# Performance work log

Measured on AMD Instinct MI355X. Metric: run time of the kernel, lower is better.

Reference implementation:

```python
import jax, jax.numpy as jnp
import numpy as np

H = 16  # num heads
D = 64  # head dim


def rotate_half(x):
    h = x.shape[-1] // 2
    return jnp.concatenate([-x[..., h:], x[..., :h]], axis=-1)


def setup_inputs() -> dict:
    key = jax.random.key(0)
    ks = jax.random.split(key, 8)
    B, S, E = 2, 4096, 1024
    scale = 1.0 / np.sqrt(E)
    x = jax.random.normal(ks[0], (B, S, E), dtype=jnp.float32)
    Wq = jax.random.normal(ks[1], (E, E), dtype=jnp.float32) * scale
    Wk = jax.random.normal(ks[2], (E, E), dtype=jnp.float32) * scale
    Wv = jax.random.normal(ks[3], (E, E), dtype=jnp.float32) * scale
    Wg = jax.random.normal(ks[4], (E, E), dtype=jnp.float32) * scale
    Wo = jax.random.normal(ks[5], (E, E), dtype=jnp.float32) * scale
    cos = jax.random.normal(ks[6], (S, D), dtype=jnp.float32)
    sin = jax.random.normal(ks[7], (S, D), dtype=jnp.float32)
    return {"x": x, "Wq": Wq, "Wk": Wk, "Wv": Wv, "Wg": Wg, "Wo": Wo,
            "cos": cos, "sin": sin, "block_size": 256}


def reference(x, Wq, Wk, Wv, Wg, Wo, cos, sin, block_size):
    B, S, E = x.shape
    nb = S // block_size  # seq divisible by block_size (remainder==0 path)

    gate = (x @ Wg).reshape(B, S, H, D)
    q = (x @ Wq).reshape(B, S, H, D)
    k = (x @ Wk).reshape(B, S, H, D)
    v = (x @ Wv).reshape(B, S, H, D)

    # RoPE: cos/sin [S, D] -> broadcast over batch and heads (unsqueeze_dim=1 in torch
    # with [S, 1, D] after slicing gives the same broadcast over the head axis here).
    c = cos[:S][None, :, None, :]  # [1, S, 1, D]
    s = sin[:S][None, :, None, :]
    q = q * c + rotate_half(q) * s
    k = k * c + rotate_half(k) * s

    # Block-diagonal attention: reshape seq into blocks and attend within blocks only.
    def to_blocks(t):  # [B,S,H,D] -> [B,nb,H,block,D]
        return t.reshape(B, nb, block_size, H, D).transpose(0, 1, 3, 2, 4)

    qb, kb, vb = to_blocks(q), to_blocks(k), to_blocks(v)
    scores = jnp.einsum('bnhqd,bnhkd->bnhqk', qb, kb) / np.sqrt(D)
    attn = jax.nn.softmax(scores, axis=-1)
    ob = jnp.einsum('bnhqk,bnhkd->bnhqd', attn, vb)

    out = ob.transpose(0, 1, 3, 2, 4).reshape(B, S, H, D)  # back to [B,S,H,D]
    out = (out * jax.nn.sigmoid(gate)).reshape(B, S, H * D)
    return out @ Wo
```

## Files before the change

### kernel.cpp

```cpp
#include <hip/hip_runtime.h>
#include <hip/hip_bf16.h>
#include <stdint.h>

typedef __bf16 bf16_t;
typedef __bf16 bf16x8 __attribute__((ext_vector_type(8)));
typedef float f32x4 __attribute__((ext_vector_type(4)));

#define DEVI __device__ __forceinline__

constexpr int BB = 2;
constexpr int SS = 4096;
constexpr int EE = 1024;
constexpr int HH = 16;
constexpr int DD = 64;
constexpr int MM = BB * SS;

DEVI void gload16(const void* g, void* l) {
  __builtin_amdgcn_global_load_lds(
      (const __attribute__((address_space(1))) void*)g,
      (__attribute__((address_space(3))) void*)l, 16, 0, 0);
}

__global__ void cvt_kernel(const float* __restrict__ in, bf16_t* __restrict__ out, int n8) {
  int i = blockIdx.x * 256 + threadIdx.x;
  if (i >= n8) return;
  const float* p = in + (size_t)i * 8;
  bf16x8 o;
#pragma unroll
  for (int j = 0; j < 8; ++j) o[j] = (bf16_t)p[j];
  *(bf16x8*)(out + (size_t)i * 8) = o;
}

__global__ void wt_kernel(const float* __restrict__ w0, const float* __restrict__ w1,
                          const float* __restrict__ w2, const float* __restrict__ w3,
                          const float* __restrict__ w4, bf16_t* __restrict__ out) {
  __shared__ float tile[32][33];
  const float* Wsel = blockIdx.z == 0 ? w0 : blockIdx.z == 1 ? w1 :
                      blockIdx.z == 2 ? w2 : blockIdx.z == 3 ? w3 : w4;
  bf16_t* O = out + (size_t)blockIdx.z * EE * EE;
  int n0 = blockIdx.x * 32, k0 = blockIdx.y * 32;
  int tx = threadIdx.x & 31, ty = threadIdx.x >> 5;
#pragma unroll
  for (int i = 0; i < 4; ++i)
    tile[ty + i * 8][tx] = Wsel[(size_t)(k0 + ty + i * 8) * EE + n0 + tx];
  __syncthreads();
#pragma unroll
  for (int i = 0; i < 4; ++i)
    O[(size_t)(n0 + ty + i * 8) * EE + k0 + tx] = (bf16_t)tile[tx][ty + i * 8];
}

template <int MODE>
__global__ __launch_bounds__(256) void gemm_bt(const bf16_t* __restrict__ A,
                                               const bf16_t* __restrict__ Bt,
                                               void* __restrict__ Cout, int Kdim) {
  __shared__ bf16_t Al[128 * 64];
  __shared__ bf16_t Bl[128 * 64];
  const int m0 = blockIdx.x * 128;
  const int n0 = blockIdx.y * 128;
  const int tid = threadIdx.x;
  const int wv = tid >> 6, ln = tid & 63;
  const int wm = wv >> 1, wn = wv & 1;
  f32x4 acc[4][4] = {};

  for (int k0 = 0; k0 < Kdim; k0 += 64) {
    __syncthreads();
#pragma unroll
    for (int i = 0; i < 4; ++i) {
      int slot = i * 256 + wv * 64 + ln;
      int r = slot >> 3, c = slot & 7;
      int cs = c ^ (r & 7);
      gload16(A + (size_t)(m0 + r) * Kdim + k0 + cs * 8, Al + (size_t)(i * 256 + wv * 64) * 8);
      gload16(Bt + (size_t)(n0 + r) * Kdim + k0 + cs * 8, Bl + (size_t)(i * 256 + wv * 64) * 8);
    }
    __syncthreads();
#pragma unroll
    for (int kk = 0; kk < 2; ++kk) {
      bf16x8 af[4], bfr[4];
#pragma unroll
      for (int mi = 0; mi < 4; ++mi) {
        int row = wm * 64 + mi * 16 + (ln & 15);
        int ch = (kk * 4 + (ln >> 4)) ^ (row & 7);
        af[mi] = *(const bf16x8*)(Al + row * 64 + ch * 8);
      }
#pragma unroll
      for (int ni = 0; ni < 4; ++ni) {
        int row = wn * 64 + ni * 16 + (ln & 15);
        int ch = (kk * 4 + (ln >> 4)) ^ (row & 7);
        bfr[ni] = *(const bf16x8*)(Bl + row * 64 + ch * 8);
      }
#pragma unroll
      for (int mi = 0; mi < 4; ++mi)
#pragma unroll
        for (int ni = 0; ni < 4; ++ni)
          acc[mi][ni] = __builtin_amdgcn_mfma_f32_16x16x32_bf16(af[mi], bfr[ni], acc[mi][ni], 0, 0, 0);
    }
  }

  if (MODE == 0) {
    bf16_t* Obase = (bf16_t*)Cout;
#pragma unroll
    for (int mi = 0; mi < 4; ++mi) {
#pragma unroll
      for (int ni = 0; ni < 4; ++ni) {
        int row = m0 + wm * 64 + mi * 16 + ((ln >> 4) << 2);
        int col = n0 + wn * 64 + ni * 16 + (ln & 15);
        int widx = col >> 10, ncol = col & 1023;
        bf16_t* W = Obase + (size_t)widx * MM * EE;
        if (widx == 2) {
          int h = ncol >> 6, d = ncol & 63;
          int b = row >> 12, s = row & (SS - 1);
          bf16_t* p = W + (((size_t)b * HH + h) * DD + d) * SS + s;
#pragma unroll
          for (int r = 0; r < 4; ++r) p[r] = (bf16_t)acc[mi][ni][r];
        } else {
          bf16_t* p = W + (size_t)row * EE + ncol;
#pragma unroll
          for (int r = 0; r < 4; ++r) p[(size_t)r * EE] = (bf16_t)acc[mi][ni][r];
        }
      }
    }
  } else {
    float* O = (float*)Cout;
#pragma unroll
    for (int mi = 0; mi < 4; ++mi)
#pragma unroll
      for (int ni = 0; ni < 4; ++ni) {
        int row = m0 + wm * 64 + mi * 16 + ((ln >> 4) << 2);
        int col = n0 + wn * 64 + ni * 16 + (ln & 15);
#pragma unroll
        for (int r = 0; r < 4; ++r) O[(size_t)(row + r) * EE + col] = acc[mi][ni][r];
      }
  }
}

__global__ __launch_bounds__(256, 2) void attn_kernel(const bf16_t* __restrict__ Q,
                                                      const bf16_t* __restrict__ Kc,
                                                      const bf16_t* __restrict__ Vt,
                                                      const bf16_t* __restrict__ G,
                                                      const float* __restrict__ cosp,
                                                      const float* __restrict__ sinp,
                                                      bf16_t* __restrict__ AO) {
  __shared__ bf16_t Kl[256 * 64];
  __shared__ bf16_t Vl[64 * 256];
  __shared__ bf16_t Pl[4][32 * 64];
  const int id = blockIdx.x;
  const int swz = (id & 7) * 128 + (id >> 3);
  const int half = swz & 1, ab = swz >> 1;
  const int h = ab & 15, sb = (ab >> 4) & 15, b = ab >> 8;
  const int tid = threadIdx.x, wv = tid >> 6, ln = tid & 63;
  const int qs0 = sb * 256 + half * 128 + wv * 32;

  {
    const bf16_t* Kbase = Kc + ((size_t)b * SS + sb * 256) * EE + h * DD;
    int kr = wv * 8 + (ln >> 3), kc8 = ln & 7;
#pragma unroll
    for (int g = 0; g < 8; ++g) {
      int r = g * 32 + kr, cs = kc8 ^ (r & 7);
      gload16(Kbase + (size_t)r * EE + cs * 8, &Kl[g * 2048 + wv * 512]);
    }
    const bf16_t* Vbase = Vt + ((size_t)b * HH + h) * DD * SS + sb * 256;
    int vr = wv * 2 + (ln >> 5), vc = ln & 31;
#pragma unroll
    for (int g = 0; g < 8; ++g) {
      int r = g * 8 + vr, cs = vc ^ ((r & 7) << 2);
      gload16(Vbase + (size_t)r * SS + cs * 8, &Vl[g * 2048 + wv * 512]);
    }
  }

  const int erow = ln >> 1, ehf = ln & 1;
  const int em = b * SS + qs0 + erow;
  bf16x8 gpre[4];
  {
    const bf16_t* gp = G + (size_t)em * EE + h * DD + ehf * 32;
#pragma unroll
    for (int i = 0; i < 4; ++i) gpre[i] = *(const bf16x8*)(gp + i * 8);
  }

  bf16x8 qraw[2][2];
  float cl[2][8], sl[2][8], chv[2][8], shv[2][8];
  const int d0 = (ln >> 4) << 3;
#pragma unroll
  for (int mi = 0; mi < 2; ++mi) {
    int qs = qs0 + mi * 16 + (ln & 15);
    const bf16_t* qp = Q + ((size_t)b * SS + qs) * EE + h * DD;
    qraw[mi][0] = *(const bf16x8*)(qp + d0);
    qraw[mi][1] = *(const bf16x8*)(qp + 32 + d0);
    *(f32x4*)&cl[mi][0] = *(const f32x4*)&cosp[qs * DD + d0];
    *(f32x4*)&cl[mi][4] = *(const f32x4*)&cosp[qs * DD + d0 + 4];
    *(f32x4*)&chv[mi][0] = *(const f32x4*)&cosp[qs * DD + d0 + 32];
    *(f32x4*)&chv[mi][4] = *(const f32x4*)&cosp[qs * DD + d0 + 36];
    *(f32x4*)&sl[mi][0] = *(const f32x4*)&sinp[qs * DD + d0];
    *(f32x4*)&sl[mi][4] = *(const f32x4*)&sinp[qs * DD + d0 + 4];
    *(f32x4*)&shv[mi][0] = *(const f32x4*)&sinp[qs * DD + d0 + 32];
    *(f32x4*)&shv[mi][4] = *(const f32x4*)&sinp[qs * DD + d0 + 36];
  }
  __syncthreads();

  bf16x8 qf[2][2];
#pragma unroll
  for (int mi = 0; mi < 2; ++mi)
#pragma unroll
    for (int j = 0; j < 8; ++j) {
      float lo = (float)qraw[mi][0][j], hi = (float)qraw[mi][1][j];
      qf[mi][0][j] = (bf16_t)(lo * cl[mi][j] - hi * sl[mi][j]);
      qf[mi][1][j] = (bf16_t)(hi * chv[mi][j] + lo * shv[mi][j]);
    }

  {
    int c_ = tid & 3;
#pragma unroll
    for (int rr = 0; rr < 4; ++rr) {
      int r_ = rr * 64 + (tid >> 2);
      int ks = sb * 256 + r_;
      int chl = ((c_ ^ (r_ & 7)) << 3), chh = (((c_ ^ 4) ^ (r_ & 7)) << 3);
      bf16x8 lo8 = *(bf16x8*)&Kl[r_ * 64 + chl];
      bf16x8 hi8 = *(bf16x8*)&Kl[r_ * 64 + chh];
      float kc_[8], ks_[8], kch[8], ksh[8];
      *(f32x4*)&kc_[0] = *(const f32x4*)&cosp[ks * DD + c_ * 8];
      *(f32x4*)&kc_[4] = *(const f32x4*)&cosp[ks * DD + c_ * 8 + 4];
      *(f32x4*)&kch[0] = *(const f32x4*)&cosp[ks * DD + c_ * 8 + 32];
      *(f32x4*)&kch[4] = *(const f32x4*)&cosp[ks * DD + c_ * 8 + 36];
      *(f32x4*)&ks_[0] = *(const f32x4*)&sinp[ks * DD + c_ * 8];
      *(f32x4*)&ks_[4] = *(const f32x4*)&sinp[ks * DD + c_ * 8 + 4];
      *(f32x4*)&ksh[0] = *(const f32x4*)&sinp[ks * DD + c_ * 8 + 32];
      *(f32x4*)&ksh[4] = *(const f32x4*)&sinp[ks * DD + c_ * 8 + 36];
      bf16x8 olo, ohi;
#pragma unroll
      for (int j = 0; j < 8; ++j) {
        float lo = (float)lo8[j], hi = (float)hi8[j];
        olo[j] = (bf16_t)(lo * kc_[j] - hi * ks_[j]);
        ohi[j] = (bf16_t)(hi * kch[j] + lo * ksh[j]);
      }
      *(bf16x8*)&Kl[r_ * 64 + chl] = olo;
      *(bf16x8*)&Kl[r_ * 64 + chh] = ohi;
    }
  }
  __syncthreads();

  f32x4 sc[2][16];
#pragma unroll
  for (int mi = 0; mi < 2; ++mi)
#pragma unroll
    for (int ni = 0; ni < 16; ++ni) sc[mi][ni] = f32x4{0.f, 0.f, 0.f, 0.f};
  __builtin_amdgcn_s_setprio(1);
#pragma unroll
  for (int kk = 0; kk < 2; ++kk) {
#pragma unroll
    for (int ni = 0; ni < 16; ++ni) {
      int row = ni * 16 + (ln & 15);
      int ch = (kk * 4 + (ln >> 4)) ^ (row & 7);
      bf16x8 kf = *(const bf16x8*)(&Kl[row * 64 + ch * 8]);
#pragma unroll
      for (int mi = 0; mi < 2; ++mi)
        sc[mi][ni] = __builtin_amdgcn_mfma_f32_16x16x32_bf16(qf[mi][kk], kf, sc[mi][ni], 0, 0, 0);
    }
  }
  __builtin_amdgcn_s_setprio(0);

  float lr[2][4];
#pragma unroll
  for (int mi = 0; mi < 2; ++mi) {
#pragma unroll
    for (int r = 0; r < 4; ++r) {
      float mx = -1e30f;
#pragma unroll
      for (int ni = 0; ni < 16; ++ni) mx = fmaxf(mx, sc[mi][ni][r] * 0.125f);
#pragma unroll
      for (int d = 1; d < 16; d <<= 1) mx = fmaxf(mx, __shfl_xor(mx, d));
      float rs = 0.f;
#pragma unroll
      for (int ni = 0; ni < 16; ++ni) {
        float p = __expf(sc[mi][ni][r] * 0.125f - mx);
        sc[mi][ni][r] = p;
        rs += p;
      }
#pragma unroll
      for (int d = 1; d < 16; d <<= 1) rs += __shfl_xor(rs, d);
      lr[mi][r] = rs;
    }
  }

  f32x4 o[2][4] = {};
  bf16_t* P = Pl[wv];
#pragma unroll
  for (int kc = 0; kc < 4; ++kc) {
#pragma unroll
    for (int mi = 0; mi < 2; ++mi)
#pragma unroll
      for (int nq = 0; nq < 4; ++nq)
#pragma unroll
        for (int r = 0; r < 4; ++r) {
          int row = mi * 16 + ((ln >> 4) << 2) + r;
          int col = nq * 16 + (ln & 15);
          P[row * 64 + (col ^ ((row & 7) << 3))] = (bf16_t)sc[mi][kc * 4 + nq][r];
        }
    __builtin_amdgcn_s_setprio(1);
#pragma unroll
    for (int kk = 0; kk < 2; ++kk) {
      bf16x8 pf[2], vf[4];
#pragma unroll
      for (int mi = 0; mi < 2; ++mi) {
        int row = mi * 16 + (ln & 15);
        int ch = (kk * 4 + (ln >> 4)) ^ (row & 7);
        pf[mi] = *(const bf16x8*)(P + row * 64 + ch * 8);
      }
#pragma unroll
      for (int nd = 0; nd < 4; ++nd) {
        int d = nd * 16 + (ln & 15);
        int c = (kc * 8 + kk * 4 + (ln >> 4)) ^ ((d & 7) << 2);
        vf[nd] = *(const bf16x8*)(&Vl[d * 256 + c * 8]);
      }
#pragma unroll
      for (int mi = 0; mi < 2; ++mi)
#pragma unroll
        for (int nd = 0; nd < 4; ++nd)
          o[mi][nd] = __builtin_amdgcn_mfma_f32_16x16x32_bf16(pf[mi], vf[nd], o[mi][nd], 0, 0, 0);
    }
    __builtin_amdgcn_s_setprio(0);
  }

  __syncthreads();
  float* lrT = (float*)Pl[wv];
  if ((ln & 15) == 0) {
#pragma unroll
    for (int mi = 0; mi < 2; ++mi)
#pragma unroll
      for (int r = 0; r < 4; ++r)
        lrT[mi * 16 + ((ln >> 4) << 2) + r] = lr[mi][r];
  }
  float* T = (float*)Kl + wv * 2048;
#pragma unroll
  for (int mi = 0; mi < 2; ++mi)
#pragma unroll
    for (int nd = 0; nd < 4; ++nd)
#pragma unroll
      for (int r = 0; r < 4; ++r) {
        int row = mi * 16 + ((ln >> 4) << 2) + r;
        int col = nd * 16 + (ln & 15);
        int c = col >> 2;
        T[row * 64 + ((c ^ (row & 7)) << 2) + (col & 3)] = o[mi][nd][r];
      }
  {
    float inv = 1.f / lrT[erow];
    f32x4 ov[8];
#pragma unroll
    for (int j = 0; j < 8; ++j) {
      int c = ehf * 8 + j;
      ov[j] = *(const f32x4*)&T[erow * 64 + ((c ^ (erow & 7)) << 2)];
    }
    bf16_t* ap = AO + (size_t)em * EE + h * DD + ehf * 32;
#pragma unroll
    for (int i = 0; i < 4; ++i) {
      bf16x8 outv;
#pragma unroll
      for (int j2 = 0; j2 < 8; ++j2) {
        float gv = (float)gpre[i][j2];
        float sig = 1.f / (1.f + __expf(-gv));
        outv[j2] = (bf16_t)(ov[i * 2 + (j2 >> 2)][j2 & 3] * inv * sig);
      }
      *(bf16x8*)(ap + i * 8) = outv;
    }
  }
}

extern "C" void kernel_launch(void* const* d_in, const int* in_sizes, int n_in,
                              void* d_out, int out_size, void* d_ws, size_t ws_size,
                              hipStream_t stream) {
  const float* x = (const float*)d_in[0];
  const float* Wq = (const float*)d_in[1];
  const float* Wk = (const float*)d_in[2];
  const float* Wv = (const float*)d_in[3];
  const float* Wg = (const float*)d_in[4];
  const float* Wo = (const float*)d_in[5];
  const float* cosp = (const float*)d_in[6];
  const float* sinp = (const float*)d_in[7];
  float* out = (float*)d_out;

  char* ws = (char*)d_ws;
  bf16_t* XB = (bf16_t*)(ws);
  bf16_t* WT = (bf16_t*)(ws + (16ll << 20));
  bf16_t* QB = (bf16_t*)(ws + (26ll << 20));
  bf16_t* KB = (bf16_t*)(ws + (42ll << 20));
  bf16_t* VT = (bf16_t*)(ws + (58ll << 20));
  bf16_t* GB = (bf16_t*)(ws + (74ll << 20));
  bf16_t* AO = XB;

  const int n8 = MM * EE / 8;
  cvt_kernel<<<n8 / 256, 256, 0, stream>>>(x, XB, n8);
  wt_kernel<<<dim3(32, 32, 5), 256, 0, stream>>>(Wq, Wk, Wv, Wg, Wo, WT);
  gemm_bt<0><<<dim3(MM / 128, 4 * EE / 128), 256, 0, stream>>>(XB, WT, QB, EE);
  attn_kernel<<<1024, 256, 0, stream>>>(QB, KB, VT, GB, cosp, sinp, AO);
  gemm_bt<1><<<dim3(MM / 128, EE / 128), 256, 0, stream>>>(AO, WT + (size_t)4 * EE * EE, out, EE);
}
```

Baseline: 155.0 us.

## Pack RoPE cos/sin to bf16 and split K/V load waits in attention

Adds a small pre-kernel that rewrites the cos/sin tables into an interleaved bf16 layout, so each thread fetches its RoPE coefficients in a few 16-byte loads instead of many fp32 loads. The attention kernel now issues those loads first, then the K and V async LDS loads, and waits only for the K loads (vmcnt(8)) before applying RoPE to K. It waits for V only right before the PV stage, so the V transfer can overlap the QK and softmax work. The cost is an extra tiny launch and bf16 rounding of cos/sin. The hand-written waitcnt counts depend on the exact instruction order, which makes the code fragile.

```diff
diff --git a/kernel.cpp b/kernel.cpp
--- a/kernel.cpp
+++ b/kernel.cpp
@@ -47,6 +47,17 @@
 #pragma unroll
   for (int i = 0; i < 4; ++i)
     O[(size_t)(n0 + ty + i * 8) * EE + k0 + tx] = (bf16_t)tile[tx][ty + i * 8];
+}
+
+__global__ void csk_kernel(const float* __restrict__ cosp, const float* __restrict__ sinp,
+                           bf16_t* __restrict__ csk) {
+  int i = blockIdx.x * 256 + threadIdx.x;
+  int s = i >> 7, idx = i & 127;
+  int c = idx >> 5, j = idx & 31;
+  int part = j >> 3, jj = j & 7;
+  int d = c * 8 + jj + ((part >= 2) ? 32 : 0);
+  const float* src = (part & 1) ? sinp : cosp;
+  csk[i] = (bf16_t)src[s * 64 + d];
 }
 
 template <int MODE>
@@ -137,8 +148,7 @@
                                                       const bf16_t* __restrict__ Kc,
                                                       const bf16_t* __restrict__ Vt,
                                                       const bf16_t* __restrict__ G,
-                                                      const float* __restrict__ cosp,
-                                                      const float* __restrict__ sinp,
+                                                      const bf16_t* __restrict__ CSK,
                                                       bf16_t* __restrict__ AO) {
   __shared__ bf16_t Kl[256 * 64];
   __shared__ bf16_t Vl[64 * 256];
@@ -150,23 +160,27 @@
   const int tid = threadIdx.x, wv = tid >> 6, ln = tid & 63;
   const int qs0 = sb * 256 + half * 128 + wv * 32;
 
-  {
-    const bf16_t* Kbase = Kc + ((size_t)b * SS + sb * 256) * EE + h * DD;
-    int kr = wv * 8 + (ln >> 3), kc8 = ln & 7;
-#pragma unroll
-    for (int g = 0; g < 8; ++g) {
-      int r = g * 32 + kr, cs = kc8 ^ (r & 7);
-      gload16(Kbase + (size_t)r * EE + cs * 8, &Kl[g * 2048 + wv * 512]);
-    }
-    const bf16_t* Vbase = Vt + ((size_t)b * HH + h) * DD * SS + sb * 256;
-    int vr = wv * 2 + (ln >> 5), vc = ln & 31;
-#pragma unroll
-    for (int g = 0; g < 8; ++g) {
-      int r = g * 8 + vr, cs = vc ^ ((r & 7) << 2);
-      gload16(Vbase + (size_t)r * SS + cs * 8, &Vl[g * 2048 + wv * 512]);
-    }
-  }
-
+  const int d0 = (ln >> 4) << 3;
+  bf16x8 qraw[2][2], qcs[2][4];
+#pragma unroll
+  for (int mi = 0; mi < 2; ++mi) {
+    int qs = qs0 + mi * 16 + (ln & 15);
+    const bf16_t* qp = Q + ((size_t)b * SS + qs) * EE + h * DD;
+    qraw[mi][0] = *(const bf16x8*)(qp + d0);
+    qraw[mi][1] = *(const bf16x8*)(qp + 32 + d0);
+    const bf16_t* cp = CSK + (size_t)qs * 128 + (d0 >> 3) * 32;
+#pragma unroll
+    for (int t = 0; t < 4; ++t) qcs[mi][t] = *(const bf16x8*)(cp + t * 8);
+  }
+  const int kcol = tid & 3;
+  bf16x8 kcs[4][4];
+#pragma unroll
+  for (int rr = 0; rr < 4; ++rr) {
+    int ks = sb * 256 + rr * 64 + (tid >> 2);
+    const bf16_t* cp = CSK + (size_t)ks * 128 + kcol * 32;
+#pragma unroll
+    for (int t = 0; t < 4; ++t) kcs[rr][t] = *(const bf16x8*)(cp + t * 8);
+  }
   const int erow = ln >> 1, ehf = ln & 1;
   const int em = b * SS + qs0 + erow;
   bf16x8 gpre[4];
@@ -175,26 +189,29 @@
 #pragma unroll
     for (int i = 0; i < 4; ++i) gpre[i] = *(const bf16x8*)(gp + i * 8);
   }
-
-  bf16x8 qraw[2][2];
-  float cl[2][8], sl[2][8], chv[2][8], shv[2][8];
-  const int d0 = (ln >> 4) << 3;
-#pragma unroll
-  for (int mi = 0; mi < 2; ++mi) {
-    int qs = qs0 + mi * 16 + (ln & 15);
-    const bf16_t* qp = Q + ((size_t)b * SS + qs) * EE + h * DD;
-    qraw[mi][0] = *(const bf16x8*)(qp + d0);
-    qraw[mi][1] = *(const bf16x8*)(qp + 32 + d0);
-    *(f32x4*)&cl[mi][0] = *(const f32x4*)&cosp[qs * DD + d0];
-    *(f32x4*)&cl[mi][4] = *(const f32x4*)&cosp[qs * DD + d0 + 4];
-    *(f32x4*)&chv[mi][0] = *(const f32x4*)&cosp[qs * DD + d0 + 32];
-    *(f32x4*)&chv[mi][4] = *(const f32x4*)&cosp[qs * DD + d0 + 36];
-    *(f32x4*)&sl[mi][0] = *(const f32x4*)&sinp[qs * DD + d0];
-    *(f32x4*)&sl[mi][4] = *(const f32x4*)&sinp[qs * DD + d0 + 4];
-    *(f32x4*)&shv[mi][0] = *(const f32x4*)&sinp[qs * DD + d0 + 32];
-    *(f32x4*)&shv[mi][4] = *(const f32x4*)&sinp[qs * DD + d0 + 36];
-  }
-  __syncthreads();
+  __builtin_amdgcn_sched_barrier(0);
+
+  {
+    const bf16_t* Kbase = Kc + ((size_t)b * SS + sb * 256) * EE + h * DD;
+    int kr = wv * 8 + (ln >> 3), kc8 = ln & 7;
+#pragma unroll
+    for (int g = 0; g < 8; ++g) {
+      int r = g * 32 + kr, cs = kc8 ^ (r & 7);
+      gload16(Kbase + (size_t)r * EE + cs * 8, &Kl[g * 2048 + wv * 512]);
+    }
+  }
+  __builtin_amdgcn_sched_barrier(0);
+
+  {
+    const bf16_t* Vbase = Vt + ((size_t)b * HH + h) * DD * SS + sb * 256;
+    int vr = wv * 2 + (ln >> 5), vc = ln & 31;
+#pragma unroll
+    for (int g = 0; g < 8; ++g) {
+      int r = g * 8 + vr, cs = vc ^ ((r & 7) << 2);
+      gload16(Vbase + (size_t)r * SS + cs * 8, &Vl[g * 2048 + wv * 512]);
+    }
+  }
+  __builtin_amdgcn_sched_barrier(0);
 
   bf16x8 qf[2][2];
 #pragma unroll
@@ -202,40 +219,34 @@
 #pragma unroll
     for (int j = 0; j < 8; ++j) {
       float lo = (float)qraw[mi][0][j], hi = (float)qraw[mi][1][j];
-      qf[mi][0][j] = (bf16_t)(lo * cl[mi][j] - hi * sl[mi][j]);
-      qf[mi][1][j] = (bf16_t)(hi * chv[mi][j] + lo * shv[mi][j]);
-    }
-
-  {
-    int c_ = tid & 3;
-#pragma unroll
-    for (int rr = 0; rr < 4; ++rr) {
-      int r_ = rr * 64 + (tid >> 2);
-      int ks = sb * 256 + r_;
-      int chl = ((c_ ^ (r_ & 7)) << 3), chh = (((c_ ^ 4) ^ (r_ & 7)) << 3);
-      bf16x8 lo8 = *(bf16x8*)&Kl[r_ * 64 + chl];
-      bf16x8 hi8 = *(bf16x8*)&Kl[r_ * 64 + chh];
-      float kc_[8], ks_[8], kch[8], ksh[8];
-      *(f32x4*)&kc_[0] = *(const f32x4*)&cosp[ks * DD + c_ * 8];
-      *(f32x4*)&kc_[4] = *(const f32x4*)&cosp[ks * DD + c_ * 8 + 4];
-      *(f32x4*)&kch[0] = *(const f32x4*)&cosp[ks * DD + c_ * 8 + 32];
-      *(f32x4*)&kch[4] = *(const f32x4*)&cosp[ks * DD + c_ * 8 + 36];
-      *(f32x4*)&ks_[0] = *(const f32x4*)&sinp[ks * DD + c_ * 8];
-      *(f32x4*)&ks_[4] = *(const f32x4*)&sinp[ks * DD + c_ * 8 + 4];
-      *(f32x4*)&ksh[0] = *(const f32x4*)&sinp[ks * DD + c_ * 8 + 32];
-      *(f32x4*)&ksh[4] = *(const f32x4*)&sinp[ks * DD + c_ * 8 + 36];
-      bf16x8 olo, ohi;
-#pragma unroll
-      for (int j = 0; j < 8; ++j) {
-        float lo = (float)lo8[j], hi = (float)hi8[j];
-        olo[j] = (bf16_t)(lo * kc_[j] - hi * ks_[j]);
-        ohi[j] = (bf16_t)(hi * kch[j] + lo * ksh[j]);
-      }
-      *(bf16x8*)&Kl[r_ * 64 + chl] = olo;
-      *(bf16x8*)&Kl[r_ * 64 + chh] = ohi;
-    }
-  }
-  __syncthreads();
+      qf[mi][0][j] = (bf16_t)(lo * (float)qcs[mi][0][j] - hi * (float)qcs[mi][1][j]);
+      qf[mi][1][j] = (bf16_t)(hi * (float)qcs[mi][2][j] + lo * (float)qcs[mi][3][j]);
+    }
+
+  asm volatile("s_waitcnt vmcnt(8)" ::: "memory");
+  __builtin_amdgcn_s_barrier();
+  __builtin_amdgcn_sched_barrier(0);
+
+#pragma unroll
+  for (int rr = 0; rr < 4; ++rr) {
+    int r_ = rr * 64 + (tid >> 2);
+    int chl = ((kcol ^ (r_ & 7)) << 3), chh = (((kcol ^ 4) ^ (r_ & 7)) << 3);
+    bf16x8 lo8 = *(bf16x8*)&Kl[r_ * 64 + chl];
+    bf16x8 hi8 = *(bf16x8*)&Kl[r_ * 64 + chh];
+    bf16x8 olo, ohi;
+#pragma unroll
+    for (int j = 0; j < 8; ++j) {
+      float lo = (float)lo8[j], hi = (float)hi8[j];
+      olo[j] = (bf16_t)(lo * (float)kcs[rr][0][j] - hi * (float)kcs[rr][1][j]);
+      ohi[j] = (bf16_t)(hi * (float)kcs[rr][2][j] + lo * (float)kcs[rr][3][j]);
+    }
+    *(bf16x8*)&Kl[r_ * 64 + chl] = olo;
+    *(bf16x8*)&Kl[r_ * 64 + chh] = ohi;
+  }
+
+  asm volatile("s_waitcnt lgkmcnt(0)" ::: "memory");
+  __builtin_amdgcn_s_barrier();
+  __builtin_amdgcn_sched_barrier(0);
 
   f32x4 sc[2][16];
 #pragma unroll
@@ -279,6 +290,10 @@
       lr[mi][r] = rs;
     }
   }
+
+  asm volatile("s_waitcnt vmcnt(0)" ::: "memory");
+  __builtin_amdgcn_s_barrier();
+  __builtin_amdgcn_sched_barrier(0);
 
   f32x4 o[2][4] = {};
   bf16_t* P = Pl[wv];
@@ -383,12 +398,14 @@
   bf16_t* KB = (bf16_t*)(ws + (42ll << 20));
   bf16_t* VT = (bf16_t*)(ws + (58ll << 20));
   bf16_t* GB = (bf16_t*)(ws + (74ll << 20));
+  bf16_t* CK = (bf16_t*)(ws + (90ll << 20));
   bf16_t* AO = XB;
 
   const int n8 = MM * EE / 8;
   cvt_kernel<<<n8 / 256, 256, 0, stream>>>(x, XB, n8);
   wt_kernel<<<dim3(32, 32, 5), 256, 0, stream>>>(Wq, Wk, Wv, Wg, Wo, WT);
+  csk_kernel<<<(SS * 128) / 256, 256, 0, stream>>>(cosp, sinp, CK);
   gemm_bt<0><<<dim3(MM / 128, 4 * EE / 128), 256, 0, stream>>>(XB, WT, QB, EE);
-  attn_kernel<<<1024, 256, 0, stream>>>(QB, KB, VT, GB, cosp, sinp, AO);
+  attn_kernel<<<1024, 256, 0, stream>>>(QB, KB, VT, GB, CK, AO);
   gemm_bt<1><<<dim3(MM / 128, EE / 128), 256, 0, stream>>>(AO, WT + (size_t)4 * EE * EE, out, EE);
 }
```

After: 155.8 us. About the same (+0.5%).
